# Performance work log

Measured on AMD Instinct MI355X. Metric: run time of the kernel, lower is better.

Reference implementation:

```python
import jax, jax.numpy as jnp
import numpy as np

B, T, NCH, NBIN, NBAND = 2, 400, 8, 512, 40
NPV = NCH * NCH


def setup_inputs() -> dict:
    key = jax.random.key(0)
    ks = jax.random.split(key, 7)
    bins_real = jax.random.normal(ks[0], (B, T, NCH, NBIN), jnp.float32)
    bins_imag = jax.random.normal(ks[1], (B, T, NCH, NBIN), jnp.float32)
    band_matrix_real = jax.random.normal(ks[2], (NBIN, NBAND), jnp.float32) * 0.05
    band_matrix_imag = jax.random.normal(ks[3], (NBIN, NBAND), jnp.float32) * 0.05
    cov_to_pv_real = jax.random.normal(ks[4], (NPV, NCH * NCH), jnp.float32) * 0.1
    cov_to_pv_imag = jax.random.normal(ks[5], (NPV, NCH * NCH), jnp.float32) * 0.1
    tau = jax.random.uniform(ks[6], (NBAND,), jnp.float32, 0.8, 0.99)
    return {
        'bins_real': bins_real, 'bins_imag': bins_imag,
        'band_matrix_real': band_matrix_real, 'band_matrix_imag': band_matrix_imag,
        'cov_to_pv_real': cov_to_pv_real, 'cov_to_pv_imag': cov_to_pv_imag,
        'tau': tau,
    }


def _power_vector(bins_real, bins_imag, band_matrix_real, band_matrix_imag,
                  cov_to_pv_real, cov_to_pv_imag, tau):
    x = jax.lax.complex(bins_real, bins_imag)            # (B,T,C,F)
    nch = x.shape[-2]
    EPS = 1e-20
    # per-bin covariance outer product, flattened cov dim: (B,T,F,C*C)
    cov = jnp.einsum('btif,btjf->btfij', x, jnp.conj(x))
    b, t, f = cov.shape[:3]
    cov = cov.reshape(b, t, f, nch * nch)
    diag = jnp.arange(nch) * (nch + 1)                   # diagonal indices in cov dim
    trace = jnp.clip(jnp.sum(cov.real[..., diag], axis=-1, keepdims=True), EPS, None)
    cov = cov / trace                                    # per-bin trace normalisation
    # phase adjustment along the bin axis (n=1 -> lag of 2 bins)
    c = jnp.swapaxes(cov, -1, -2)                        # (B,T,C2,F)
    prod = jnp.conj(c[..., :-2]) * c[..., 2:]
    ang = jnp.arctan2(prod.imag, prod.real)
    ang = jnp.concatenate([ang[..., :1], ang, ang[..., -1:]], axis=-1)  # edge pad
    adj = jnp.abs(c) * jax.lax.complex(jnp.cos(ang), jnp.sin(ang))
    adj = adj.at[..., diag, :].set(c[..., diag, :])      # keep original diagonals
    # band projection: contract bins against (F,K) band matrix
    bm = jax.lax.complex(band_matrix_real, band_matrix_imag)
    band_cov = jnp.einsum('btcf,fk->btkc', adj, bm)      # (B,T,K,C2)
    dsum = jnp.clip(band_cov.real[..., diag].sum(-1, keepdims=True), EPS, None)
    band_cov = band_cov / dsum
    # first-order IIR smoothing over frames, per-band pole tau
    a = tau[:, None].astype(band_cov.real.dtype)         # (K,1)
    def step(carry, xt):
        y = a * carry + (1.0 - a) * xt
        return y, y
    y0 = jnp.zeros_like(band_cov[:, 0])                  # (B,K,C2)
    _, ys = jax.lax.scan(step, y0, jnp.moveaxis(band_cov, 1, 0))
    band_cov = jnp.moveaxis(ys, 0, 1)                    # (B,T,K,C2)
    # cov -> power vector projection, real part
    c2p = jax.lax.complex(cov_to_pv_real, cov_to_pv_imag)  # (P,C2)
    pv = jnp.einsum('pc,btkc->btkp', c2p, band_cov).real   # (B,T,K,P)
    return pv


def reference(bins_real, bins_imag, band_matrix_real, band_matrix_imag,
              cov_to_pv_real, cov_to_pv_imag, tau):
    return _power_vector(bins_real, bins_imag, band_matrix_real, band_matrix_imag,
                         cov_to_pv_real, cov_to_pv_imag, tau)
```

## Files before the change

### kernel.cpp

```cpp
#include <hip/hip_runtime.h>
#include <hip/hip_fp16.h>

#define B_    2
#define T_    400
#define NCH_  8
#define NBIN_ 512
#define NBAND_ 40
#define NPV_  64

using half8   = __attribute__((ext_vector_type(8))) _Float16;
using float4v = __attribute__((ext_vector_type(4))) float;

static __device__ inline unsigned pkhf(float x, float y) {
  __half2 h = __float22half2_rn(make_float2(x, y));
  return __builtin_bit_cast(unsigned, h);
}
static __device__ inline unsigned rot16(unsigned u) {
  return (u >> 16) | (u << 16);
}
static __device__ inline unsigned cmulc(unsigned viu, unsigned vju) {
  __half2 Vi = __builtin_bit_cast(__half2, viu);
  __half2 Vj = __builtin_bit_cast(__half2, vju);
  __half2 P1 = __hmul2(Vi, __low2half2(Vj));
  __half2 Qi = __lowhigh2highlow(Vi);
  unsigned tn = __builtin_bit_cast(unsigned, __high2half2(Vj)) ^ 0x80000000u;
  __half2 a  = __hfma2(Qi, __builtin_bit_cast(__half2, tn), P1);
  return __builtin_bit_cast(unsigned, a);
}
static __device__ inline void gld_lds16(const uint4* g, uint4* l) {
  auto* lds_ptr = reinterpret_cast<__attribute__((address_space(3))) uint4*>(
      reinterpret_cast<uintptr_t>(l));
  auto* g_ptr = reinterpret_cast<const __attribute__((address_space(1))) uint4*>(
      reinterpret_cast<uintptr_t>(g));
  __builtin_amdgcn_global_load_lds(g_ptr, lds_ptr, 16, 0, 0);
}

__global__ __launch_bounds__(256) void pv_prep(
    const float* __restrict__ bmr, const float* __restrict__ bmi,
    const float* __restrict__ c2pr, const float* __restrict__ c2pi,
    float* __restrict__ ws)
{
  const int tid = threadIdx.x;
  const int blk = blockIdx.x;
  if (blk == 0) {
    __shared__ float sds[256];
    int k = tid & 63, part = tid >> 6;
    float s = 0.f;
    if (k < NBAND_) {
      const float* col = bmr + k;
      #pragma unroll 16
      for (int f = part * 128; f < part * 128 + 128; f++) s += col[f * 40];
    }
    sds[tid] = s;
    __syncthreads();
    if (tid < NBAND_) {
      float t = sds[tid] + sds[tid + 64] + sds[tid + 128] + sds[tid + 192];
      ws[tid] = 1.0f / fmaxf(t, 1e-20f);
    }
  } else if (blk <= 24) {
    int F = (blk - 1) * 256 + tid;
    int l = F & 63;
    int fid = F >> 6;
    int s5 = fid / 3;
    int n = fid - s5 * 3;
    int k = n * 16 + (l & 15);
    int quad = l >> 4;
    unsigned dw[4];
    #pragma unroll
    for (int t2 = 0; t2 < 4; t2++) {
      float v0 = 0.f, v1 = 0.f;
      if (k < NBAND_) {
        int f = s5 * 16 + quad * 4 + t2;
        v0 = bmr[f * 40 + k]; v1 = bmi[f * 40 + k];
      }
      dw[t2] = pkhf(v0, v1);
    }
    ((uint4*)((char*)ws + 1024))[F] = make_uint4(dw[0], dw[1], dw[2], dw[3]);
  } else {
    int F2 = (blk - 25) * 256 + tid;
    int lane = F2 & 63, E = F2 >> 6;
    int nt = E >> 2, ks = E & 3;
    int n = lane & 15, quad = lane >> 4;
    int p = nt * 16 + n;
    unsigned dw[4];
    #pragma unroll
    for (int t2 = 0; t2 < 4; t2++) {
      int c = ks * 16 + quad * 4 + t2;
      dw[t2] = pkhf(c2pr[p * 64 + c], -c2pi[p * 64 + c]);
    }
    ((uint4*)((char*)ws + 197632))[E * 64 + lane] = make_uint4(dw[0], dw[1], dw[2], dw[3]);
  }
}

__global__ __launch_bounds__(256, 4) void pv_main(
    const float* __restrict__ br, const float* __restrict__ bi,
    const float* __restrict__ ws, float* __restrict__ out)
{
  __shared__ __align__(16) unsigned smem[10240];
  unsigned* vsh = smem;
  uint4*    bst = (uint4*)(smem + 4096);

  const int bt  = blockIdx.x;
  const int tid = threadIdx.x;
  const float* pr  = br + (size_t)bt * (NCH_ * NBIN_);
  const float* pim = bi + (size_t)bt * (NCH_ * NBIN_);

  const int mt   = tid >> 6;
  const int lane = tid & 63;
  const int m16  = lane & 15;
  const int quad = lane >> 4;
  const int p    = mt * 16 + m16;
  const int ich  = p >> 3, jch = p & 7;
  const uint4* BF0 = (const uint4*)((const char*)ws + 1024);

  {
    const uint4* g = BF0 + tid;
    uint4* l = bst + tid;
    gld_lds16(g, l);
    gld_lds16(g + 256, l + 256);
    gld_lds16(g + 512, l + 512);
  }

  #pragma unroll
  for (int fs = 0; fs < 2; fs++) {
    const int f = fs * 256 + tid;
    const int fm = (f == 0) ? 0 : ((f == 511) ? 509 : f - 1);
    const int fp = (f == 0) ? 2 : ((f == 511) ? 511 : f + 1);
    float tr = 0.f;
    float t1[8], t2[8];
    #pragma unroll
    for (int c = 0; c < 8; c++) {
      const float* cr = pr + c * 512;
      const float* ci = pim + c * 512;
      float xr = cr[f],   xi = ci[f];
      float xrm = cr[fm], xim = ci[fm];
      float xrp = cr[fp], xip = ci[fp];
      tr = fmaf(xr, xr, tr); tr = fmaf(xi, xi, tr);
      float Gr = fmaf(xrm, xrp,  xim * xip);
      float Gi = fmaf(xrm, xip, -(xim * xrp));
      float am = fmaxf(fmaxf(fabsf(Gr), fabsf(Gi)), 1e-30f);
      float rc = __builtin_amdgcn_rcpf(am);
      float q1 = Gr * rc, q2 = Gi * rc;
      float n2 = fmaf(q1, q1, q2 * q2);
      float rn = __builtin_amdgcn_rsqf(n2);
      bool ok = n2 > 0.f;
      float ur = ok ? q1 * rn : 1.f;
      float ui = ok ? q2 * rn : 0.f;
      float mg = __builtin_amdgcn_sqrtf(fmaf(xr, xr, xi * xi));
      t1[c] = mg * ur; t2[c] = mg * ui;
    }
    float scv = __builtin_amdgcn_rsqf(fmaxf(tr, 1e-20f));
    const int fc = f >> 2, fl = f & 3;
    #pragma unroll
    for (int c = 0; c < 8; c++)
      vsh[c * 512 + ((fc ^ c) << 2) + fl] = pkhf(t1[c] * scv, t2[c] * scv);
  }
  __syncthreads();

  const uint4* vb = (const uint4*)vsh;

  float4v acc[6];
  #pragma unroll
  for (int g = 0; g < 6; g++) acc[g] = (float4v){0.f, 0.f, 0.f, 0.f};

  for (int st = 0; st < 8; st++) {
    if (st < 7) {
      const uint4* g = BF0 + (st + 1) * 768 + tid;
      uint4* l = bst + ((st + 1) & 1) * 768 + tid;
      gld_lds16(g, l);
      gld_lds16(g + 256, l + 256);
      gld_lds16(g + 512, l + 512);
    }
    const uint4* bb = bst + (st & 1) * 768;
    #pragma unroll
    for (int q = 0; q < 4; q++) {
      const int s = st * 4 + q;
      const int sc = s * 4 + quad;
      uint4 av = vb[ich * 128 + (sc ^ ich)];
      uint4 bv = vb[jch * 128 + (sc ^ jch)];
      uint4 cb0 = bb[(q * 3 + 0) * 64 + lane];
      uint4 cb1 = bb[(q * 3 + 1) * 64 + lane];
      uint4 cb2 = bb[(q * 3 + 2) * 64 + lane];
      unsigned a0 = cmulc(av.x, bv.x);
      unsigned a1 = cmulc(av.y, bv.y);
      unsigned a2 = cmulc(av.z, bv.z);
      unsigned a3 = cmulc(av.w, bv.w);
      uint4 au1 = make_uint4(a0 ^ 0x80000000u, a1 ^ 0x80000000u,
                             a2 ^ 0x80000000u, a3 ^ 0x80000000u);
      uint4 au2 = make_uint4(rot16(a0), rot16(a1),
                             rot16(a2), rot16(a3));
      half8 af1 = __builtin_bit_cast(half8, au1);
      half8 af2 = __builtin_bit_cast(half8, au2);
      half8 b0 = __builtin_bit_cast(half8, cb0);
      half8 b1 = __builtin_bit_cast(half8, cb1);
      half8 b2 = __builtin_bit_cast(half8, cb2);
      acc[0] = __builtin_amdgcn_mfma_f32_16x16x32_f16(af1, b0, acc[0], 0, 0, 0);
      acc[3] = __builtin_amdgcn_mfma_f32_16x16x32_f16(af2, b0, acc[3], 0, 0, 0);
      acc[1] = __builtin_amdgcn_mfma_f32_16x16x32_f16(af1, b1, acc[1], 0, 0, 0);
      acc[4] = __builtin_amdgcn_mfma_f32_16x16x32_f16(af2, b1, acc[4], 0, 0, 0);
      acc[2] = __builtin_amdgcn_mfma_f32_16x16x32_f16(af1, b2, acc[2], 0, 0, 0);
      acc[5] = __builtin_amdgcn_mfma_f32_16x16x32_f16(af2, b2, acc[5], 0, 0, 0);
    }
    __syncthreads();
  }

  const uint4* EF = ((const uint4*)((const char*)ws + 197632)) + (mt * 4) * 64 + lane;
  uint4 eb[4];
  #pragma unroll
  for (int ks = 0; ks < 4; ks++) eb[ks] = EF[ks * 64];

  unsigned* bcsh = smem;
  #pragma unroll
  for (int n = 0; n < 3; n++) {
    uint4 w4 = make_uint4(pkhf(acc[n][0], acc[n + 3][0]),
                          pkhf(acc[n][1], acc[n + 3][1]),
                          pkhf(acc[n][2], acc[n + 3][2]),
                          pkhf(acc[n][3], acc[n + 3][3]));
    *(uint4*)(bcsh + (n * 16 + m16) * 68 + mt * 16 + quad * 4) = w4;
  }
  __syncthreads();

  float4v eacc[3];
  #pragma unroll
  for (int kt = 0; kt < 3; kt++) eacc[kt] = (float4v){0.f, 0.f, 0.f, 0.f};
  #pragma unroll
  for (int ks = 0; ks < 4; ks++) {
    half8 bfr = __builtin_bit_cast(half8, eb[ks]);
    #pragma unroll
    for (int kt = 0; kt < 3; kt++) {
      uint4 a4 = *(const uint4*)(bcsh + (kt * 16 + m16) * 68 + ks * 16 + quad * 4);
      half8 afr = __builtin_bit_cast(half8, a4);
      eacc[kt] = __builtin_amdgcn_mfma_f32_16x16x32_f16(afr, bfr, eacc[kt], 0, 0, 0);
    }
  }
  float* op = out + (size_t)bt * (NBAND_ * NPV_);
  const float4* wsd = (const float4*)ws;
  #pragma unroll
  for (int kt = 0; kt < 3; kt++) {
    float4 dv = wsd[kt * 4 + quad];
    float dva[4] = {dv.x, dv.y, dv.z, dv.w};
    #pragma unroll
    for (int r = 0; r < 4; r++) {
      int k = kt * 16 + quad * 4 + r;
      if (k < NBAND_)
        op[k * 64 + mt * 16 + m16] = eacc[kt][r] * dva[r];
    }
  }
}

__global__ __launch_bounds__(256) void pv_iir3(float* __restrict__ z,
                                               const float* __restrict__ tau)
{
  __shared__ float gsh[16][16];
  const int pg = blockIdx.x & 3;
  const int bk = blockIdx.x >> 2;
  const int k = bk % NBAND_;
  const int b = bk / NBAND_;
  const float a  = tau[k];
  const float om = 1.0f - a;
  const int c  = threadIdx.x >> 4;
  const int pl = threadIdx.x & 15;
  const int p  = pg * 16 + pl;
  const size_t stride = (size_t)NBAND_ * 64;
  size_t idx0 = (size_t)b * (T_ * NBAND_ * 64) + (size_t)(c * 25) * stride + k * 64 + p;

  float y[25];
  float accv = 0.f;
  #pragma unroll
  for (int i = 0; i < 25; i++) {
    float v = z[idx0 + (size_t)i * stride];
    accv = fmaf(a, accv, om * v);
    y[i] = accv;
  }
  gsh[c][pl] = accv;
  __syncthreads();
  float a2 = a * a, a8 = a2 * a2 * a2 * a2, a16 = a8 * a8;
  float A = a16 * a8 * a;
  float H = 0.f;
  #pragma unroll
  for (int d = 0; d < 15; d++) {
    if (d < c) H = fmaf(A, H, gsh[d][pl]);
  }
  float wp = a;
  #pragma unroll
  for (int i = 0; i < 25; i++) {
    z[idx0 + (size_t)i * stride] = fmaf(wp, H, y[i]);
    wp *= a;
  }
}

extern "C" void kernel_launch(void* const* d_in, const int* in_sizes, int n_in,
                              void* d_out, int out_size, void* d_ws, size_t ws_size,
                              hipStream_t stream)
{
  const float* br   = (const float*)d_in[0];
  const float* bi   = (const float*)d_in[1];
  const float* bmr  = (const float*)d_in[2];
  const float* bmi  = (const float*)d_in[3];
  const float* c2pr = (const float*)d_in[4];
  const float* c2pi = (const float*)d_in[5];
  const float* tau  = (const float*)d_in[6];
  float* out = (float*)d_out;
  float* ws  = (float*)d_ws;

  hipLaunchKernelGGL(pv_prep, dim3(29), dim3(256), 0, stream,
                     bmr, bmi, c2pr, c2pi, ws);
  hipLaunchKernelGGL(pv_main, dim3(B_ * T_), dim3(256), 0, stream,
                     br, bi, ws, out);
  hipLaunchKernelGGL(pv_iir3, dim3(B_ * NBAND_ * 4), dim3(256), 0, stream,
                     out, tau);
}
```

Baseline: 114.0 us.

## Process two frames per block in main kernel and widen IIR scan chunks

The main kernel now handles two (b,t) frames per block, so each band-matrix tile streamed into shared memory is reused by both frames' MFMAs. This halves the band-matrix traffic and the grid size, at the cost of more registers, more shared memory and lower occupancy (launch bounds drop to 2). The IIR kernel splits time into 40 chunks of 10 frames with 640 threads instead of 16 chunks of 25, which shortens each thread's serial chain but lengthens the prefix combine loop.

Result: no change. 113.1 us (-0.8%).

```diff
diff --git a/kernel.cpp b/kernel.cpp
--- a/kernel.cpp
+++ b/kernel.cpp
@@ -92,18 +92,16 @@
   }
 }
 
-__global__ __launch_bounds__(256, 4) void pv_main(
+__global__ __launch_bounds__(256, 2) void pv_main(
     const float* __restrict__ br, const float* __restrict__ bi,
     const float* __restrict__ ws, float* __restrict__ out)
 {
-  __shared__ __align__(16) unsigned smem[10240];
-  unsigned* vsh = smem;
-  uint4*    bst = (uint4*)(smem + 4096);
-
-  const int bt  = blockIdx.x;
+  __shared__ __align__(16) unsigned smem[14336];
+  unsigned* vshA[2] = { smem, smem + 4096 };
+  uint4*    bst = (uint4*)(smem + 8192);
+
+  const int bt0 = blockIdx.x * 2;
   const int tid = threadIdx.x;
-  const float* pr  = br + (size_t)bt * (NCH_ * NBIN_);
-  const float* pim = bi + (size_t)bt * (NCH_ * NBIN_);
 
   const int mt   = tid >> 6;
   const int lane = tid & 63;
@@ -122,46 +120,50 @@
   }
 
   #pragma unroll
-  for (int fs = 0; fs < 2; fs++) {
-    const int f = fs * 256 + tid;
-    const int fm = (f == 0) ? 0 : ((f == 511) ? 509 : f - 1);
-    const int fp = (f == 0) ? 2 : ((f == 511) ? 511 : f + 1);
-    float tr = 0.f;
-    float t1[8], t2[8];
-    #pragma unroll
-    for (int c = 0; c < 8; c++) {
-      const float* cr = pr + c * 512;
-      const float* ci = pim + c * 512;
-      float xr = cr[f],   xi = ci[f];
-      float xrm = cr[fm], xim = ci[fm];
-      float xrp = cr[fp], xip = ci[fp];
-      tr = fmaf(xr, xr, tr); tr = fmaf(xi, xi, tr);
-      float Gr = fmaf(xrm, xrp,  xim * xip);
-      float Gi = fmaf(xrm, xip, -(xim * xrp));
-      float am = fmaxf(fmaxf(fabsf(Gr), fabsf(Gi)), 1e-30f);
-      float rc = __builtin_amdgcn_rcpf(am);
-      float q1 = Gr * rc, q2 = Gi * rc;
-      float n2 = fmaf(q1, q1, q2 * q2);
-      float rn = __builtin_amdgcn_rsqf(n2);
-      bool ok = n2 > 0.f;
-      float ur = ok ? q1 * rn : 1.f;
-      float ui = ok ? q2 * rn : 0.f;
-      float mg = __builtin_amdgcn_sqrtf(fmaf(xr, xr, xi * xi));
-      t1[c] = mg * ur; t2[c] = mg * ui;
-    }
-    float scv = __builtin_amdgcn_rsqf(fmaxf(tr, 1e-20f));
-    const int fc = f >> 2, fl = f & 3;
-    #pragma unroll
-    for (int c = 0; c < 8; c++)
-      vsh[c * 512 + ((fc ^ c) << 2) + fl] = pkhf(t1[c] * scv, t2[c] * scv);
+  for (int h = 0; h < 2; h++) {
+    const float* pr  = br + (size_t)(bt0 + h) * (NCH_ * NBIN_);
+    const float* pim = bi + (size_t)(bt0 + h) * (NCH_ * NBIN_);
+    unsigned* vsh = vshA[h];
+    #pragma unroll
+    for (int fs = 0; fs < 2; fs++) {
+      const int f = fs * 256 + tid;
+      const int fm = (f == 0) ? 0 : ((f == 511) ? 509 : f - 1);
+      const int fp = (f == 0) ? 2 : ((f == 511) ? 511 : f + 1);
+      float tr = 0.f;
+      float t1[8], t2[8];
+      #pragma unroll
+      for (int c = 0; c < 8; c++) {
+        const float* cr = pr + c * 512;
+        const float* ci = pim + c * 512;
+        float xr = cr[f],   xi = ci[f];
+        float xrm = cr[fm], xim = ci[fm];
+        float xrp = cr[fp], xip = ci[fp];
+        tr = fmaf(xr, xr, tr); tr = fmaf(xi, xi, tr);
+        float Gr = fmaf(xrm, xrp,  xim * xip);
+        float Gi = fmaf(xrm, xip, -(xim * xrp));
+        float am = fmaxf(fmaxf(fabsf(Gr), fabsf(Gi)), 1e-30f);
+        float rc = __builtin_amdgcn_rcpf(am);
+        float q1 = Gr * rc, q2 = Gi * rc;
+        float n2 = fmaf(q1, q1, q2 * q2);
+        float rn = __builtin_amdgcn_rsqf(n2);
+        bool ok = n2 > 0.f;
+        float ur = ok ? q1 * rn : 1.f;
+        float ui = ok ? q2 * rn : 0.f;
+        float mg = __builtin_amdgcn_sqrtf(fmaf(xr, xr, xi * xi));
+        t1[c] = mg * ur; t2[c] = mg * ui;
+      }
+      float scv = __builtin_amdgcn_rsqf(fmaxf(tr, 1e-20f));
+      const int fc = f >> 2, fl = f & 3;
+      #pragma unroll
+      for (int c = 0; c < 8; c++)
+        vsh[c * 512 + ((fc ^ c) << 2) + fl] = pkhf(t1[c] * scv, t2[c] * scv);
+    }
   }
   __syncthreads();
 
-  const uint4* vb = (const uint4*)vsh;
-
-  float4v acc[6];
-  #pragma unroll
-  for (int g = 0; g < 6; g++) acc[g] = (float4v){0.f, 0.f, 0.f, 0.f};
+  float4v acc[12];
+  #pragma unroll
+  for (int g = 0; g < 12; g++) acc[g] = (float4v){0.f, 0.f, 0.f, 0.f};
 
   for (int st = 0; st < 8; st++) {
     if (st < 7) {
@@ -176,30 +178,34 @@
     for (int q = 0; q < 4; q++) {
       const int s = st * 4 + q;
       const int sc = s * 4 + quad;
-      uint4 av = vb[ich * 128 + (sc ^ ich)];
-      uint4 bv = vb[jch * 128 + (sc ^ jch)];
       uint4 cb0 = bb[(q * 3 + 0) * 64 + lane];
       uint4 cb1 = bb[(q * 3 + 1) * 64 + lane];
       uint4 cb2 = bb[(q * 3 + 2) * 64 + lane];
-      unsigned a0 = cmulc(av.x, bv.x);
-      unsigned a1 = cmulc(av.y, bv.y);
-      unsigned a2 = cmulc(av.z, bv.z);
-      unsigned a3 = cmulc(av.w, bv.w);
-      uint4 au1 = make_uint4(a0 ^ 0x80000000u, a1 ^ 0x80000000u,
-                             a2 ^ 0x80000000u, a3 ^ 0x80000000u);
-      uint4 au2 = make_uint4(rot16(a0), rot16(a1),
-                             rot16(a2), rot16(a3));
-      half8 af1 = __builtin_bit_cast(half8, au1);
-      half8 af2 = __builtin_bit_cast(half8, au2);
       half8 b0 = __builtin_bit_cast(half8, cb0);
       half8 b1 = __builtin_bit_cast(half8, cb1);
       half8 b2 = __builtin_bit_cast(half8, cb2);
-      acc[0] = __builtin_amdgcn_mfma_f32_16x16x32_f16(af1, b0, acc[0], 0, 0, 0);
-      acc[3] = __builtin_amdgcn_mfma_f32_16x16x32_f16(af2, b0, acc[3], 0, 0, 0);
-      acc[1] = __builtin_amdgcn_mfma_f32_16x16x32_f16(af1, b1, acc[1], 0, 0, 0);
-      acc[4] = __builtin_amdgcn_mfma_f32_16x16x32_f16(af2, b1, acc[4], 0, 0, 0);
-      acc[2] = __builtin_amdgcn_mfma_f32_16x16x32_f16(af1, b2, acc[2], 0, 0, 0);
-      acc[5] = __builtin_amdgcn_mfma_f32_16x16x32_f16(af2, b2, acc[5], 0, 0, 0);
+      #pragma unroll
+      for (int h = 0; h < 2; h++) {
+        const uint4* vb = (const uint4*)vshA[h];
+        uint4 av = vb[ich * 128 + (sc ^ ich)];
+        uint4 bv = vb[jch * 128 + (sc ^ jch)];
+        unsigned a0 = cmulc(av.x, bv.x);
+        unsigned a1 = cmulc(av.y, bv.y);
+        unsigned a2 = cmulc(av.z, bv.z);
+        unsigned a3 = cmulc(av.w, bv.w);
+        uint4 au1 = make_uint4(a0 ^ 0x80000000u, a1 ^ 0x80000000u,
+                               a2 ^ 0x80000000u, a3 ^ 0x80000000u);
+        uint4 au2 = make_uint4(rot16(a0), rot16(a1),
+                               rot16(a2), rot16(a3));
+        half8 af1 = __builtin_bit_cast(half8, au1);
+        half8 af2 = __builtin_bit_cast(half8, au2);
+        acc[h*6+0] = __builtin_amdgcn_mfma_f32_16x16x32_f16(af1, b0, acc[h*6+0], 0, 0, 0);
+        acc[h*6+3] = __builtin_amdgcn_mfma_f32_16x16x32_f16(af2, b0, acc[h*6+3], 0, 0, 0);
+        acc[h*6+1] = __builtin_amdgcn_mfma_f32_16x16x32_f16(af1, b1, acc[h*6+1], 0, 0, 0);
+        acc[h*6+4] = __builtin_amdgcn_mfma_f32_16x16x32_f16(af2, b1, acc[h*6+4], 0, 0, 0);
+        acc[h*6+2] = __builtin_amdgcn_mfma_f32_16x16x32_f16(af1, b2, acc[h*6+2], 0, 0, 0);
+        acc[h*6+5] = __builtin_amdgcn_mfma_f32_16x16x32_f16(af2, b2, acc[h*6+5], 0, 0, 0);
+      }
     }
     __syncthreads();
   }
@@ -209,49 +215,56 @@
   #pragma unroll
   for (int ks = 0; ks < 4; ks++) eb[ks] = EF[ks * 64];
 
-  unsigned* bcsh = smem;
-  #pragma unroll
-  for (int n = 0; n < 3; n++) {
-    uint4 w4 = make_uint4(pkhf(acc[n][0], acc[n + 3][0]),
-                          pkhf(acc[n][1], acc[n + 3][1]),
-                          pkhf(acc[n][2], acc[n + 3][2]),
-                          pkhf(acc[n][3], acc[n + 3][3]));
-    *(uint4*)(bcsh + (n * 16 + m16) * 68 + mt * 16 + quad * 4) = w4;
+  #pragma unroll
+  for (int h = 0; h < 2; h++) {
+    unsigned* bcsh = vshA[h];
+    #pragma unroll
+    for (int n = 0; n < 3; n++) {
+      uint4 w4 = make_uint4(pkhf(acc[h*6+n][0], acc[h*6+n+3][0]),
+                            pkhf(acc[h*6+n][1], acc[h*6+n+3][1]),
+                            pkhf(acc[h*6+n][2], acc[h*6+n+3][2]),
+                            pkhf(acc[h*6+n][3], acc[h*6+n+3][3]));
+      *(uint4*)(bcsh + (n * 16 + m16) * 68 + mt * 16 + quad * 4) = w4;
+    }
   }
   __syncthreads();
 
-  float4v eacc[3];
-  #pragma unroll
-  for (int kt = 0; kt < 3; kt++) eacc[kt] = (float4v){0.f, 0.f, 0.f, 0.f};
-  #pragma unroll
-  for (int ks = 0; ks < 4; ks++) {
-    half8 bfr = __builtin_bit_cast(half8, eb[ks]);
+  const float4* wsd = (const float4*)ws;
+  #pragma unroll
+  for (int h = 0; h < 2; h++) {
+    const unsigned* bcsh = vshA[h];
+    float4v eacc[3];
+    #pragma unroll
+    for (int kt = 0; kt < 3; kt++) eacc[kt] = (float4v){0.f, 0.f, 0.f, 0.f};
+    #pragma unroll
+    for (int ks = 0; ks < 4; ks++) {
+      half8 bfr = __builtin_bit_cast(half8, eb[ks]);
+      #pragma unroll
+      for (int kt = 0; kt < 3; kt++) {
+        uint4 a4 = *(const uint4*)(bcsh + (kt * 16 + m16) * 68 + ks * 16 + quad * 4);
+        half8 afr = __builtin_bit_cast(half8, a4);
+        eacc[kt] = __builtin_amdgcn_mfma_f32_16x16x32_f16(afr, bfr, eacc[kt], 0, 0, 0);
+      }
+    }
+    float* op = out + (size_t)(bt0 + h) * (NBAND_ * NPV_);
     #pragma unroll
     for (int kt = 0; kt < 3; kt++) {
-      uint4 a4 = *(const uint4*)(bcsh + (kt * 16 + m16) * 68 + ks * 16 + quad * 4);
-      half8 afr = __builtin_bit_cast(half8, a4);
-      eacc[kt] = __builtin_amdgcn_mfma_f32_16x16x32_f16(afr, bfr, eacc[kt], 0, 0, 0);
-    }
-  }
-  float* op = out + (size_t)bt * (NBAND_ * NPV_);
-  const float4* wsd = (const float4*)ws;
-  #pragma unroll
-  for (int kt = 0; kt < 3; kt++) {
-    float4 dv = wsd[kt * 4 + quad];
-    float dva[4] = {dv.x, dv.y, dv.z, dv.w};
-    #pragma unroll
-    for (int r = 0; r < 4; r++) {
-      int k = kt * 16 + quad * 4 + r;
-      if (k < NBAND_)
-        op[k * 64 + mt * 16 + m16] = eacc[kt][r] * dva[r];
-    }
-  }
-}
-
-__global__ __launch_bounds__(256) void pv_iir3(float* __restrict__ z,
+      float4 dv = wsd[kt * 4 + quad];
+      float dva[4] = {dv.x, dv.y, dv.z, dv.w};
+      #pragma unroll
+      for (int r = 0; r < 4; r++) {
+        int k = kt * 16 + quad * 4 + r;
+        if (k < NBAND_)
+          op[k * 64 + mt * 16 + m16] = eacc[kt][r] * dva[r];
+      }
+    }
+  }
+}
+
+__global__ __launch_bounds__(640) void pv_iir4(float* __restrict__ z,
                                                const float* __restrict__ tau)
 {
-  __shared__ float gsh[16][16];
+  __shared__ float gsh[40][16];
   const int pg = blockIdx.x & 3;
   const int bk = blockIdx.x >> 2;
   const int k = bk % NBAND_;
@@ -262,28 +275,29 @@
   const int pl = threadIdx.x & 15;
   const int p  = pg * 16 + pl;
   const size_t stride = (size_t)NBAND_ * 64;
-  size_t idx0 = (size_t)b * (T_ * NBAND_ * 64) + (size_t)(c * 25) * stride + k * 64 + p;
-
-  float y[25];
+  size_t idx0 = (size_t)b * (T_ * NBAND_ * 64) + (size_t)(c * 10) * stride + k * 64 + p;
+
+  float y[10];
   float accv = 0.f;
   #pragma unroll
-  for (int i = 0; i < 25; i++) {
+  for (int i = 0; i < 10; i++) {
     float v = z[idx0 + (size_t)i * stride];
     accv = fmaf(a, accv, om * v);
     y[i] = accv;
   }
   gsh[c][pl] = accv;
   __syncthreads();
-  float a2 = a * a, a8 = a2 * a2 * a2 * a2, a16 = a8 * a8;
-  float A = a16 * a8 * a;
+  float a2 = a * a, a4 = a2 * a2, a8 = a4 * a4;
+  float A = a8 * a2;
   float H = 0.f;
   #pragma unroll
-  for (int d = 0; d < 15; d++) {
-    if (d < c) H = fmaf(A, H, gsh[d][pl]);
+  for (int d = 0; d < 39; d++) {
+    float g = gsh[d][pl];
+    H = (d < c) ? fmaf(A, H, g) : H;
   }
   float wp = a;
   #pragma unroll
-  for (int i = 0; i < 25; i++) {
+  for (int i = 0; i < 10; i++) {
     z[idx0 + (size_t)i * stride] = fmaf(wp, H, y[i]);
     wp *= a;
   }
@@ -305,8 +319,8 @@
 
   hipLaunchKernelGGL(pv_prep, dim3(29), dim3(256), 0, stream,
                      bmr, bmi, c2pr, c2pi, ws);
-  hipLaunchKernelGGL(pv_main, dim3(B_ * T_), dim3(256), 0, stream,
+  hipLaunchKernelGGL(pv_main, dim3(B_ * T_ / 2), dim3(256), 0, stream,
                      br, bi, ws, out);
-  hipLaunchKernelGGL(pv_iir3, dim3(B_ * NBAND_ * 4), dim3(256), 0, stream,
+  hipLaunchKernelGGL(pv_iir4, dim3(B_ * NBAND_ * 4), dim3(640), 0, stream,
                      out, tau);
 }
```
